# Optimization experiments

Hardware: AMD Instinct MI355X
Metric: run time of the kernel (lower is better)

Reference implementation:

```python
import jax, jax.numpy as jnp
import numpy as np

D_MODEL = 1024
N_HEAD = 16
D_HEAD = D_MODEL // N_HEAD
B, S = 4, 2048


def setup_inputs() -> dict:
    key = jax.random.key(0)
    ks = jax.random.split(key, 9)
    s = 1.0 / np.sqrt(D_MODEL)
    inp = {"x": jax.random.normal(ks[0], (B, S, D_MODEL), dtype=jnp.float32)}
    for i, name in enumerate(["q", "k", "v", "o"]):
        inp[f"W{name}"] = jax.random.uniform(ks[1 + 2 * i], (D_MODEL, D_MODEL), jnp.float32, -s, s)
        inp[f"b{name}"] = jax.random.uniform(ks[2 + 2 * i], (D_MODEL,), jnp.float32, -s, s)
    return inp


def reference(x, Wq, bq, Wk, bk, Wv, bv, Wo, bo):
    b, sq, _ = x.shape
    skv = sq
    # projections (torch Linear: x @ W^T + b), reshape to (b, h, s, d)
    def proj(W, bias):
        return (x @ W.T + bias).reshape(b, sq, N_HEAD, D_HEAD).transpose(0, 2, 1, 3)
    q, k, v = proj(Wq, bq), proj(Wk, bk), proj(Wv, bv)
    scale = np.sqrt(D_HEAD).astype(np.float32)
    scores = jnp.einsum("bhqd,bhkd->bhqk", q, k) / scale
    causal_mask = jnp.triu(jnp.ones((sq, skv), dtype=bool), k=1)
    scores = jnp.where(causal_mask, -jnp.inf, scores)
    attn = jax.nn.softmax(scores, axis=-1)
    o = jnp.einsum("bhqk,bhkd->bhqd", attn, v)  # (b, h, sq, d_head)
    o = o.transpose(0, 2, 1, 3).reshape(b, sq, D_MODEL)
    return o @ Wo.T + bo
```

## Files before the change

### kernel.cpp

```cpp
#include <hip/hip_runtime.h>
#include <hip/hip_bf16.h>
#include <math.h>

#define S_LEN 2048
#define DMODEL 1024
#define NHEAD 16
#define DHEAD 64
#define BATCH 4
#define MROWS (BATCH * S_LEN)

typedef unsigned short u16;
typedef __attribute__((ext_vector_type(4))) unsigned short u16x4;
typedef __attribute__((ext_vector_type(8))) unsigned short u16x8;
typedef __attribute__((ext_vector_type(2))) unsigned u32x2;
typedef __attribute__((ext_vector_type(4))) unsigned u32x4;
typedef __attribute__((ext_vector_type(8))) short bf16x8;
typedef __attribute__((ext_vector_type(4))) float f32x4;

#define GLDS16(g, l)                                              \
  __builtin_amdgcn_global_load_lds(                               \
      (const __attribute__((address_space(1))) void*)(g),         \
      (__attribute__((address_space(3))) void*)(l), 16, 0, 0)

__device__ __forceinline__ u16 f2bf(float f) {
  unsigned u = __float_as_uint(f);
  u += 0x7fff + ((u >> 16) & 1);
  return (u16)(u >> 16);
}

__device__ __forceinline__ unsigned pkbf2(float lo, float hi) {
  __hip_bfloat162 h = __float22bfloat162_rn(float2{lo, hi});
  unsigned r;
  __builtin_memcpy(&r, &h, 4);
  return r;
}

__device__ __forceinline__ float exp2v(float x) {
  float r;
  asm("v_exp_f32 %0, %1" : "=v"(r) : "v"(x));
  return r;
}

__device__ __forceinline__ f32x4 mfma16(bf16x8 a, bf16x8 b, f32x4 c) {
  return __builtin_amdgcn_mfma_f32_16x16x32_bf16(a, b, c, 0, 0, 0);
}

__global__ __launch_bounds__(256) void castall(
    const float* __restrict__ x,
    const float* __restrict__ w0, const float* __restrict__ w1,
    const float* __restrict__ w2, const float* __restrict__ w3,
    u16* __restrict__ ox,
    u16* __restrict__ o0, u16* __restrict__ o1,
    u16* __restrict__ o2, u16* __restrict__ o3) {
  const int blk = blockIdx.x;
  const float* in;
  u16* out;
  int base;
  if (blk < 4096)      { in = x;  out = ox; base = blk; }
  else if (blk < 4608) { in = w0; out = o0; base = blk - 4096; }
  else if (blk < 5120) { in = w1; out = o1; base = blk - 4608; }
  else if (blk < 5632) { in = w2; out = o2; base = blk - 5120; }
  else                 { in = w3; out = o3; base = blk - 5632; }
  const int i = (base * 256 + threadIdx.x) * 8;
  f32x4 v0 = *(const f32x4*)(in + i);
  f32x4 v1 = *(const f32x4*)(in + i + 4);
  u16x8 o;
#pragma unroll
  for (int j = 0; j < 4; ++j) { o[j] = f2bf(v0[j]); o[4 + j] = f2bf(v1[j]); }
  *(u16x8*)(out + i) = o;
}

__global__ __launch_bounds__(256) void gemm_qkv(
    const u16* __restrict__ Xb,
    const u16* __restrict__ W0, const u16* __restrict__ W1, const u16* __restrict__ W2,
    const float* __restrict__ b0, const float* __restrict__ b1, const float* __restrict__ b2,
    u16* __restrict__ O0, u16* __restrict__ O1, u16* __restrict__ O2) {
  __shared__ u16 As[128 * 64];
  __shared__ u16 Bs[128 * 64];
  const int flat = blockIdx.x;
  const int xcd = flat & 7, idx = flat >> 3;
  const int ymt = xcd * 8 + idx / 24;
  const int rem = idx % 24;
  const int xnt = rem & 7;
  const int z = rem >> 3;
  const u16* Wm = z == 0 ? W0 : (z == 1 ? W1 : W2);
  const float* bias = z == 0 ? b0 : (z == 1 ? b1 : b2);
  u16* Out = z == 0 ? O0 : (z == 1 ? O1 : O2);
  const float qs = (z == 0) ? 0.18033688011112042f : 1.0f;
  const int tid = threadIdx.x;
  const int wave = tid >> 6, lane = tid & 63, g = lane >> 4, c = lane & 15;
  const int wm = wave >> 1, wn = wave & 1;
  const int bm0 = ymt * 128, bn0 = xnt * 128;

  f32x4 acc[4][4];
#pragma unroll
  for (int m = 0; m < 4; ++m)
#pragma unroll
    for (int n = 0; n < 4; ++n) acc[m][n] = (f32x4){0.f, 0.f, 0.f, 0.f};

  for (int k0 = 0; k0 < DMODEL; k0 += 64) {
    __syncthreads();
#pragma unroll
    for (int cc = 0; cc < 4; ++cc) {
      const int ci = cc * 256 + tid;
      const int row = ci >> 3, ch = ci & 7;
      const int sc = ((ch ^ (row & 7)) << 3);
      GLDS16(Xb + (size_t)(bm0 + row) * DMODEL + k0 + sc,
             (char*)As + (cc * 256 + wave * 64) * 16);
      GLDS16(Wm + (size_t)(bn0 + row) * DMODEL + k0 + sc,
             (char*)Bs + (cc * 256 + wave * 64) * 16);
    }
    __syncthreads();
#pragma unroll
    for (int ks = 0; ks < 2; ++ks) {
      bf16x8 af[4], bfr[4];
#pragma unroll
      for (int m = 0; m < 4; ++m) {
        const int arow = wm * 64 + m * 16 + c;
        af[m] = *(const bf16x8*)((const char*)As + arow * 128 +
                                 (((ks * 4 + g) ^ (arow & 7)) << 4));
      }
#pragma unroll
      for (int n = 0; n < 4; ++n) {
        const int brow = wn * 64 + n * 16 + c;
        bfr[n] = *(const bf16x8*)((const char*)Bs + brow * 128 +
                                  (((ks * 4 + g) ^ (brow & 7)) << 4));
      }
#pragma unroll
      for (int m = 0; m < 4; ++m)
#pragma unroll
        for (int n = 0; n < 4; ++n)
          acc[m][n] = mfma16(af[m], bfr[n], acc[m][n]);
    }
  }
  if (z < 2) {
#pragma unroll
    for (int n = 0; n < 4; ++n) {
      const int coln = bn0 + wn * 64 + n * 16 + c;
      const float bn_ = bias[coln];
      const int h = coln >> 6, d = coln & 63;
#pragma unroll
      for (int m = 0; m < 4; ++m) {
#pragma unroll
        for (int r = 0; r < 4; ++r) {
          const int rowm = bm0 + wm * 64 + m * 16 + g * 4 + r;
          const int b_ = rowm >> 11, s_ = rowm & 2047;
          Out[(((size_t)(b_ * NHEAD + h) * S_LEN + s_) << 6) + d] =
              f2bf((acc[m][n][r] + bn_) * qs);
        }
      }
    }
  } else {
#pragma unroll
    for (int n = 0; n < 4; ++n) {
      const int coln = bn0 + wn * 64 + n * 16 + c;
      const float bn_ = bias[coln];
      const int h = coln >> 6, d = coln & 63;
#pragma unroll
      for (int m = 0; m < 4; ++m) {
        const int row0 = bm0 + wm * 64 + m * 16 + g * 4;
        const int b_ = row0 >> 11, s_ = row0 & 2047;
        u16x4 pk;
#pragma unroll
        for (int r = 0; r < 4; ++r) pk[r] = f2bf(acc[m][n][r] + bn_);
        *(u16x4*)(Out + ((size_t)(b_ * NHEAD + h) * DHEAD + d) * S_LEN + s_) = pk;
      }
    }
  }
}

__global__ __launch_bounds__(256) void gemm_out(
    const u16* __restrict__ Ab, const u16* __restrict__ Wm,
    const float* __restrict__ bias, float* __restrict__ Out) {
  __shared__ u16 As[128 * 64];
  __shared__ u16 Bs[128 * 64];
  const int flat = blockIdx.x;
  const int xcd = flat & 7, idx = flat >> 3;
  const int ymt = xcd * 8 + (idx >> 3);
  const int xnt = idx & 7;
  const int tid = threadIdx.x;
  const int wave = tid >> 6, lane = tid & 63, g = lane >> 4, c = lane & 15;
  const int wm = wave >> 1, wn = wave & 1;
  const int bm0 = ymt * 128, bn0 = xnt * 128;

  f32x4 acc[4][4];
#pragma unroll
  for (int m = 0; m < 4; ++m)
#pragma unroll
    for (int n = 0; n < 4; ++n) acc[m][n] = (f32x4){0.f, 0.f, 0.f, 0.f};

  for (int k0 = 0; k0 < DMODEL; k0 += 64) {
    __syncthreads();
#pragma unroll
    for (int cc = 0; cc < 4; ++cc) {
      const int ci = cc * 256 + tid;
      const int row = ci >> 3, ch = ci & 7;
      const int sc = ((ch ^ (row & 7)) << 3);
      GLDS16(Ab + (size_t)(bm0 + row) * DMODEL + k0 + sc,
             (char*)As + (cc * 256 + wave * 64) * 16);
      GLDS16(Wm + (size_t)(bn0 + row) * DMODEL + k0 + sc,
             (char*)Bs + (cc * 256 + wave * 64) * 16);
    }
    __syncthreads();
#pragma unroll
    for (int ks = 0; ks < 2; ++ks) {
      bf16x8 af[4], bfr[4];
#pragma unroll
      for (int m = 0; m < 4; ++m) {
        const int arow = wm * 64 + m * 16 + c;
        af[m] = *(const bf16x8*)((const char*)As + arow * 128 +
                                 (((ks * 4 + g) ^ (arow & 7)) << 4));
      }
#pragma unroll
      for (int n = 0; n < 4; ++n) {
        const int brow = wn * 64 + n * 16 + c;
        bfr[n] = *(const bf16x8*)((const char*)Bs + brow * 128 +
                                  (((ks * 4 + g) ^ (brow & 7)) << 4));
      }
#pragma unroll
      for (int m = 0; m < 4; ++m)
#pragma unroll
        for (int n = 0; n < 4; ++n)
          acc[m][n] = mfma16(af[m], bfr[n], acc[m][n]);
    }
  }
#pragma unroll
  for (int n = 0; n < 4; ++n) {
    const int coln = bn0 + wn * 64 + n * 16 + c;
    const float bn_ = bias[coln];
#pragma unroll
    for (int m = 0; m < 4; ++m) {
#pragma unroll
      for (int r = 0; r < 4; ++r) {
        const int rowm = bm0 + wm * 64 + m * 16 + g * 4 + r;
        Out[(size_t)rowm * DMODEL + coln] = acc[m][n][r] + bn_;
      }
    }
  }
}

__global__ __launch_bounds__(256) void attn_fwd(const u16* __restrict__ Qb,
                                                const u16* __restrict__ Kb,
                                                const u16* __restrict__ VTb,
                                                u16* __restrict__ AOb) {
  __shared__ u16 Kt[64 * 64];
  __shared__ u16 Vt[64 * 64];
  __shared__ unsigned Pl[4][16 * 36];
  const int tid = threadIdx.x;
  const int w = tid >> 6, lane = tid & 63, g = lane >> 4, c = lane & 15;
  const int flat = blockIdx.x;
  const int xcd = flat & 7, idx = flat >> 3;
  const int qt = 31 - (idx >> 3);
  const int bh = xcd * 8 + (idx & 7);
  const size_t base = (size_t)bh * (S_LEN * DHEAD);
  const int b_ = bh >> 4, h = bh & 15;
  const int ci0 = w * 64 + lane;

  const int row0_ = ci0 >> 3,            colg0 = (ci0 & 7) ^ (row0_ & 7);
  const int row1_ = (256 + ci0) >> 3,    colg1 = ((256 + ci0) & 7) ^ (row1_ & 7);

  const int qb = qt * 64;
  const int q = qb + w * 16 + c;
  const bf16x8 qf0 = *(const bf16x8*)(Qb + base + (size_t)q * 64 + g * 8);
  const bf16x8 qf1 = *(const bf16x8*)(Qb + base + (size_t)q * 64 + 32 + g * 8);

  f32x4 oacc[4];
#pragma unroll
  for (int dt = 0; dt < 4; ++dt) oacc[dt] = (f32x4){0.f, 0.f, 0.f, 0.f};
  float m = -30000.f, l = 0.f;

  u32x4 kreg0, kreg1, vreg0, vreg1;
#define STAGE_LOAD(kt_) do {                                                  \
    const int kv0_ = (kt_) * 64;                                              \
    kreg0 = *(const u32x4*)(Kb + base + (size_t)(kv0_ + row0_) * 64 + colg0 * 8); \
    vreg0 = *(const u32x4*)(VTb + base + (size_t)row0_ * S_LEN + kv0_ + colg0 * 8); \
    kreg1 = *(const u32x4*)(Kb + base + (size_t)(kv0_ + row1_) * 64 + colg1 * 8); \
    vreg1 = *(const u32x4*)(VTb + base + (size_t)row1_ * S_LEN + kv0_ + colg1 * 8); \
  } while (0)

  const int nt = qt + 1;
  STAGE_LOAD(0);
  for (int kt = 0; kt < nt; ++kt) {
    const int kv0 = kt * 64;
    __syncthreads();
    *(u32x4*)((char*)Kt + ci0 * 16) = kreg0;
    *(u32x4*)((char*)Vt + ci0 * 16) = vreg0;
    *(u32x4*)((char*)Kt + (256 + ci0) * 16) = kreg1;
    *(u32x4*)((char*)Vt + (256 + ci0) * 16) = vreg1;
    __syncthreads();
    if (kt + 1 < nt) STAGE_LOAD(kt + 1);

    f32x4 s[4];
    __builtin_amdgcn_s_setprio(1);
#pragma unroll
    for (int t = 0; t < 4; ++t) {
      const int krow = t * 16 + c;
      const char* kbase = (const char*)Kt + krow * 128;
      bf16x8 kf0 = *(const bf16x8*)(kbase + ((g ^ (krow & 7)) * 16));
      bf16x8 kf1 = *(const bf16x8*)(kbase + (((4 + g) ^ (krow & 7)) * 16));
      f32x4 zacc = (f32x4){0.f, 0.f, 0.f, 0.f};
      zacc = mfma16(kf0, qf0, zacc);
      zacc = mfma16(kf1, qf1, zacc);
      s[t] = zacc;
    }
    __builtin_amdgcn_s_setprio(0);
    if (kt == nt - 1) {
#pragma unroll
      for (int t = 0; t < 4; ++t)
#pragma unroll
        for (int r = 0; r < 4; ++r)
          if (kv0 + t * 16 + 4 * g + r > q) s[t][r] = -30000.f;
    }
    const float a0 = fmaxf(fmaxf(s[0][0], s[0][1]), s[0][2]);
    const float a1 = fmaxf(fmaxf(s[0][3], s[1][0]), s[1][1]);
    const float a2 = fmaxf(fmaxf(s[1][2], s[1][3]), s[2][0]);
    const float a3 = fmaxf(fmaxf(s[2][1], s[2][2]), s[2][3]);
    const float a4 = fmaxf(fmaxf(s[3][0], s[3][1]), s[3][2]);
    float pm = fmaxf(fmaxf(fmaxf(a0, a1), a2), fmaxf(fmaxf(a3, a4), s[3][3]));
    pm = fmaxf(pm, __shfl_xor(pm, 16));
    pm = fmaxf(pm, __shfl_xor(pm, 32));
    if (__any(pm > m + 8.0f)) {
      const float mn = fmaxf(m, pm);
      const float sc = exp2v(m - mn);
      l *= sc;
#pragma unroll
      for (int dt = 0; dt < 4; ++dt) oacc[dt] *= sc;
      m = mn;
    }
    float rs = 0.f;
#pragma unroll
    for (int t = 0; t < 4; ++t) {
      const float p0 = exp2v(s[t][0] - m), p1 = exp2v(s[t][1] - m);
      const float p2 = exp2v(s[t][2] - m), p3 = exp2v(s[t][3] - m);
      rs += (p0 + p1) + (p2 + p3);
      u32x2 pk2;
      pk2[0] = pkbf2(p0, p1);
      pk2[1] = pkbf2(p2, p3);
      *(u32x2*)&Pl[w][c * 36 + t * 8 + g * 2] = pk2;
    }
    rs += __shfl_xor(rs, 16);
    rs += __shfl_xor(rs, 32);
    l += rs;

    __builtin_amdgcn_s_setprio(1);
#pragma unroll
    for (int kk = 0; kk < 2; ++kk) {
      const bf16x8 pb = *(const bf16x8*)&Pl[w][c * 36 + kk * 16 + g * 4];
#pragma unroll
      for (int dt = 0; dt < 4; ++dt) {
        const int vrow = dt * 16 + c;
        const bf16x8 vf = *(const bf16x8*)((const char*)Vt + vrow * 128 +
                                           (((kk * 4 + g) ^ (vrow & 7)) * 16));
        oacc[dt] = mfma16(vf, pb, oacc[dt]);
      }
    }
    __builtin_amdgcn_s_setprio(0);
  }
#undef STAGE_LOAD
  const float inv = 1.0f / l;
  const size_t rowbase = ((size_t)(b_ * S_LEN + q) * DMODEL) + h * 64;
#pragma unroll
  for (int dt = 0; dt < 4; ++dt) {
    u16x4 pk4;
#pragma unroll
    for (int r = 0; r < 4; ++r) pk4[r] = f2bf(oacc[dt][r] * inv);
    *(u16x4*)(AOb + rowbase + dt * 16 + 4 * g) = pk4;
  }
}

extern "C" void kernel_launch(void* const* d_in, const int* in_sizes, int n_in,
                              void* d_out, int out_size, void* d_ws, size_t ws_size,
                              hipStream_t stream) {
  const float* x  = (const float*)d_in[0];
  const float* Wq = (const float*)d_in[1];
  const float* bq = (const float*)d_in[2];
  const float* Wk = (const float*)d_in[3];
  const float* bk = (const float*)d_in[4];
  const float* Wv = (const float*)d_in[5];
  const float* bv = (const float*)d_in[6];
  const float* Wo = (const float*)d_in[7];
  const float* bo = (const float*)d_in[8];
  float* out = (float*)d_out;
  char* ws = (char*)d_ws;

  const size_t MB = 1024 * 1024;
  u16* xb  = (u16*)(ws);
  u16* Wqb = (u16*)(ws + 16 * MB);
  u16* Wkb = (u16*)(ws + 18 * MB);
  u16* Wvb = (u16*)(ws + 20 * MB);
  u16* Wob = (u16*)(ws + 22 * MB);
  u16* Qb  = (u16*)(ws + 24 * MB);
  u16* Kb  = (u16*)(ws + 40 * MB);
  u16* VTb = (u16*)(ws + 56 * MB);
  u16* AOb = (u16*)(ws + 72 * MB);

  castall<<<6144, 256, 0, stream>>>(x, Wq, Wk, Wv, Wo, xb, Wqb, Wkb, Wvb, Wob);

  gemm_qkv<<<1536, 256, 0, stream>>>(
      xb, Wqb, Wkb, Wvb, bq, bk, bv, Qb, Kb, VTb);

  attn_fwd<<<2048, 256, 0, stream>>>(Qb, Kb, VTb, AOb);

  gemm_out<<<512, 256, 0, stream>>>(AOb, Wob, bo, out);
}
```

Before: 177.8 us.

## Prefetch GEMM tiles through registers instead of direct global-to-LDS loads

```diff
diff --git a/kernel.cpp b/kernel.cpp
--- a/kernel.cpp
+++ b/kernel.cpp
@@ -16,11 +16,6 @@
 typedef __attribute__((ext_vector_type(4))) unsigned u32x4;
 typedef __attribute__((ext_vector_type(8))) short bf16x8;
 typedef __attribute__((ext_vector_type(4))) float f32x4;
-
-#define GLDS16(g, l)                                              \
-  __builtin_amdgcn_global_load_lds(                               \
-      (const __attribute__((address_space(1))) void*)(g),         \
-      (__attribute__((address_space(3))) void*)(l), 16, 0, 0)
 
 __device__ __forceinline__ u16 f2bf(float f) {
   unsigned u = __float_as_uint(f);
@@ -88,29 +83,50 @@
   u16* Out = z == 0 ? O0 : (z == 1 ? O1 : O2);
   const float qs = (z == 0) ? 0.18033688011112042f : 1.0f;
   const int tid = threadIdx.x;
-  const int wave = tid >> 6, lane = tid & 63, g = lane >> 4, c = lane & 15;
+  const int lane = tid & 63, g = lane >> 4, c = lane & 15;
+  const int wave = tid >> 6;
   const int wm = wave >> 1, wn = wave & 1;
   const int bm0 = ymt * 128, bn0 = xnt * 128;
 
+  int srow[4], scol[4];
+#pragma unroll
+  for (int cc = 0; cc < 4; ++cc) {
+    const int ci = cc * 256 + tid;
+    srow[cc] = ci >> 3;
+    scol[cc] = ((ci & 7) ^ (srow[cc] & 7)) << 3;
+  }
+
   f32x4 acc[4][4];
 #pragma unroll
   for (int m = 0; m < 4; ++m)
 #pragma unroll
     for (int n = 0; n < 4; ++n) acc[m][n] = (f32x4){0.f, 0.f, 0.f, 0.f};
 
+  u32x4 ar0, ar1, ar2, ar3, br0, br1, br2, br3;
+#define GLOAD(k0_) do {                                                        \
+    ar0 = *(const u32x4*)(Xb + (size_t)(bm0 + srow[0]) * DMODEL + (k0_) + scol[0]); \
+    br0 = *(const u32x4*)(Wm + (size_t)(bn0 + srow[0]) * DMODEL + (k0_) + scol[0]); \
+    ar1 = *(const u32x4*)(Xb + (size_t)(bm0 + srow[1]) * DMODEL + (k0_) + scol[1]); \
+    br1 = *(const u32x4*)(Wm + (size_t)(bn0 + srow[1]) * DMODEL + (k0_) + scol[1]); \
+    ar2 = *(const u32x4*)(Xb + (size_t)(bm0 + srow[2]) * DMODEL + (k0_) + scol[2]); \
+    br2 = *(const u32x4*)(Wm + (size_t)(bn0 + srow[2]) * DMODEL + (k0_) + scol[2]); \
+    ar3 = *(const u32x4*)(Xb + (size_t)(bm0 + srow[3]) * DMODEL + (k0_) + scol[3]); \
+    br3 = *(const u32x4*)(Wm + (size_t)(bn0 + srow[3]) * DMODEL + (k0_) + scol[3]); \
+  } while (0)
+
+  GLOAD(0);
   for (int k0 = 0; k0 < DMODEL; k0 += 64) {
     __syncthreads();
-#pragma unroll
-    for (int cc = 0; cc < 4; ++cc) {
-      const int ci = cc * 256 + tid;
-      const int row = ci >> 3, ch = ci & 7;
-      const int sc = ((ch ^ (row & 7)) << 3);
-      GLDS16(Xb + (size_t)(bm0 + row) * DMODEL + k0 + sc,
-             (char*)As + (cc * 256 + wave * 64) * 16);
-      GLDS16(Wm + (size_t)(bn0 + row) * DMODEL + k0 + sc,
-             (char*)Bs + (cc * 256 + wave * 64) * 16);
-    }
-    __syncthreads();
+    *(u32x4*)((char*)As + (0 * 256 + tid) * 16) = ar0;
+    *(u32x4*)((char*)Bs + (0 * 256 + tid) * 16) = br0;
+    *(u32x4*)((char*)As + (1 * 256 + tid) * 16) = ar1;
+    *(u32x4*)((char*)Bs + (1 * 256 + tid) * 16) = br1;
+    *(u32x4*)((char*)As + (2 * 256 + tid) * 16) = ar2;
+    *(u32x4*)((char*)Bs + (2 * 256 + tid) * 16) = br2;
+    *(u32x4*)((char*)As + (3 * 256 + tid) * 16) = ar3;
+    *(u32x4*)((char*)Bs + (3 * 256 + tid) * 16) = br3;
+    __syncthreads();
+    if (k0 + 64 < DMODEL) GLOAD(k0 + 64);
 #pragma unroll
     for (int ks = 0; ks < 2; ++ks) {
       bf16x8 af[4], bfr[4];
@@ -133,6 +149,7 @@
           acc[m][n] = mfma16(af[m], bfr[n], acc[m][n]);
     }
   }
+#undef GLOAD
   if (z < 2) {
 #pragma unroll
     for (int n = 0; n < 4; ++n) {
@@ -179,29 +196,50 @@
   const int ymt = xcd * 8 + (idx >> 3);
   const int xnt = idx & 7;
   const int tid = threadIdx.x;
-  const int wave = tid >> 6, lane = tid & 63, g = lane >> 4, c = lane & 15;
+  const int lane = tid & 63, g = lane >> 4, c = lane & 15;
+  const int wave = tid >> 6;
   const int wm = wave >> 1, wn = wave & 1;
   const int bm0 = ymt * 128, bn0 = xnt * 128;
 
+  int srow[4], scol[4];
+#pragma unroll
+  for (int cc = 0; cc < 4; ++cc) {
+    const int ci = cc * 256 + tid;
+    srow[cc] = ci >> 3;
+    scol[cc] = ((ci & 7) ^ (srow[cc] & 7)) << 3;
+  }
+
   f32x4 acc[4][4];
 #pragma unroll
   for (int m = 0; m < 4; ++m)
 #pragma unroll
     for (int n = 0; n < 4; ++n) acc[m][n] = (f32x4){0.f, 0.f, 0.f, 0.f};
 
+  u32x4 ar0, ar1, ar2, ar3, br0, br1, br2, br3;
+#define GLOAD(k0_) do {                                                        \
+    ar0 = *(const u32x4*)(Ab + (size_t)(bm0 + srow[0]) * DMODEL + (k0_) + scol[0]); \
+    br0 = *(const u32x4*)(Wm + (size_t)(bn0 + srow[0]) * DMODEL + (k0_) + scol[0]); \
+    ar1 = *(const u32x4*)(Ab + (size_t)(bm0 + srow[1]) * DMODEL + (k0_) + scol[1]); \
+    br1 = *(const u32x4*)(Wm + (size_t)(bn0 + srow[1]) * DMODEL + (k0_) + scol[1]); \
+    ar2 = *(const u32x4*)(Ab + (size_t)(bm0 + srow[2]) * DMODEL + (k0_) + scol[2]); \
+    br2 = *(const u32x4*)(Wm + (size_t)(bn0 + srow[2]) * DMODEL + (k0_) + scol[2]); \
+    ar3 = *(const u32x4*)(Ab + (size_t)(bm0 + srow[3]) * DMODEL + (k0_) + scol[3]); \
+    br3 = *(const u32x4*)(Wm + (size_t)(bn0 + srow[3]) * DMODEL + (k0_) + scol[3]); \
+  } while (0)
+
+  GLOAD(0);
   for (int k0 = 0; k0 < DMODEL; k0 += 64) {
     __syncthreads();
-#pragma unroll
-    for (int cc = 0; cc < 4; ++cc) {
-      const int ci = cc * 256 + tid;
-      const int row = ci >> 3, ch = ci & 7;
-      const int sc = ((ch ^ (row & 7)) << 3);
-      GLDS16(Ab + (size_t)(bm0 + row) * DMODEL + k0 + sc,
-             (char*)As + (cc * 256 + wave * 64) * 16);
-      GLDS16(Wm + (size_t)(bn0 + row) * DMODEL + k0 + sc,
-             (char*)Bs + (cc * 256 + wave * 64) * 16);
-    }
-    __syncthreads();
+    *(u32x4*)((char*)As + (0 * 256 + tid) * 16) = ar0;
+    *(u32x4*)((char*)Bs + (0 * 256 + tid) * 16) = br0;
+    *(u32x4*)((char*)As + (1 * 256 + tid) * 16) = ar1;
+    *(u32x4*)((char*)Bs + (1 * 256 + tid) * 16) = br1;
+    *(u32x4*)((char*)As + (2 * 256 + tid) * 16) = ar2;
+    *(u32x4*)((char*)Bs + (2 * 256 + tid) * 16) = br2;
+    *(u32x4*)((char*)As + (3 * 256 + tid) * 16) = ar3;
+    *(u32x4*)((char*)Bs + (3 * 256 + tid) * 16) = br3;
+    __syncthreads();
+    if (k0 + 64 < DMODEL) GLOAD(k0 + 64);
 #pragma unroll
     for (int ks = 0; ks < 2; ++ks) {
       bf16x8 af[4], bfr[4];
@@ -224,6 +262,7 @@
           acc[m][n] = mfma16(af[m], bfr[n], acc[m][n]);
     }
   }
+#undef GLOAD
 #pragma unroll
   for (int n = 0; n < 4; ++n) {
     const int coln = bn0 + wn * 64 + n * 16 + c;
@@ -291,7 +330,6 @@
     if (kt + 1 < nt) STAGE_LOAD(kt + 1);
 
     f32x4 s[4];
-    __builtin_amdgcn_s_setprio(1);
 #pragma unroll
     for (int t = 0; t < 4; ++t) {
       const int krow = t * 16 + c;
@@ -303,7 +341,6 @@
       zacc = mfma16(kf1, qf1, zacc);
       s[t] = zacc;
     }
-    __builtin_amdgcn_s_setprio(0);
     if (kt == nt - 1) {
 #pragma unroll
       for (int t = 0; t < 4; ++t)
@@ -342,7 +379,6 @@
     rs += __shfl_xor(rs, 32);
     l += rs;
 
-    __builtin_amdgcn_s_setprio(1);
 #pragma unroll
     for (int kk = 0; kk < 2; ++kk) {
       const bf16x8 pb = *(const bf16x8*)&Pl[w][c * 36 + kk * 16 + g * 4];
@@ -354,7 +390,6 @@
         oacc[dt] = mfma16(vf, pb, oacc[dt]);
       }
     }
-    __builtin_amdgcn_s_setprio(0);
   }
 #undef STAGE_LOAD
   const float inv = 1.0f / l;
```

Result: faster. 171.5 us (-3.5%).
